# Kernel optimization log

Hardware: AMD Instinct MI355X
Metric: run time of the kernel (lower is better)

Reference implementation:

```python
import jax, jax.numpy as jnp
import numpy as np

N, K, M, DIM = 131072, 16, 128, 64


def setup_inputs() -> dict:
    key = jax.random.key(0)
    kx, ks, ka, kb = jax.random.split(key, 4)
    return {
        "x": jax.random.normal(kx, (N, DIM), dtype=jnp.float32),
        "s": jax.random.normal(ks, (K,), dtype=jnp.float32),
        "a": jax.random.normal(ka, (K, M, DIM), dtype=jnp.float32),
        "b": jax.random.normal(kb, (K, M), dtype=jnp.float32),
    }


def reference(x, s, a, b):
    # scores[k, n, m] = x[n, :] @ a[k, m, :] + b[k, m]  (batched GEMM over k)
    scores = jnp.einsum("nd,kmd->knm", x, a) + b[:, None, :]
    # per-expert logsumexp over the m affine pieces -> [k, n]
    lse = jax.nn.logsumexp(scores, axis=-1)
    # signed sum over experts -> [n]
    return jnp.einsum("k,kn->n", s, lse)
```

## Files before the change

kernel.cpp:

```cpp
#include <hip/hip_runtime.h>
#include <hip/hip_bf16.h>

#define NROWS 131072
#define KEXP 16
#define MPC 128
#define DIMD 64

typedef float f32x4  __attribute__((ext_vector_type(4)));
typedef float f32x16 __attribute__((ext_vector_type(16)));
typedef short s16x8  __attribute__((ext_vector_type(8)));

#define L2E 1.4426950408889634f
#define LN2 0.6931471805599453f

static __device__ inline unsigned int b2u(__hip_bfloat162 h) {
    union { __hip_bfloat162 h; unsigned int u; } c;
    c.h = h;
    return c.u;
}

static __device__ inline int4 cvt8s(float4 f0, float4 f1, float sc) {
    __hip_bfloat162 p0 = __float22bfloat162_rn(make_float2(f0.x * sc, f0.y * sc));
    __hip_bfloat162 p1 = __float22bfloat162_rn(make_float2(f0.z * sc, f0.w * sc));
    __hip_bfloat162 p2 = __float22bfloat162_rn(make_float2(f1.x * sc, f1.y * sc));
    __hip_bfloat162 p3 = __float22bfloat162_rn(make_float2(f1.z * sc, f1.w * sc));
    int4 pk;
    pk.x = (int)b2u(p0); pk.y = (int)b2u(p1); pk.z = (int)b2u(p2); pk.w = (int)b2u(p3);
    return pk;
}

static __device__ inline void async_copy16(const void* g, void* l) {
    __builtin_amdgcn_global_load_lds(
        (const __attribute__((address_space(1))) unsigned int*)g,
        (__attribute__((address_space(3))) unsigned int*)l, 16, 0, 0);
}

__global__ void prep_kernel(const float* __restrict__ a, const float* __restrict__ b,
                            short* __restrict__ abff) {
    const int u   = blockIdx.x * 256 + threadIdx.x;
    const int k   = u / 1280;
    const int rem = u - k * 1280;
    const int mt  = rem / 320;
    const int rc  = rem - mt * 320;
    const int c   = rc >> 6;
    const int ul  = rc & 63;
    int4 pk;
    if (c < 4) {
        const float* p = a + (size_t)(k * MPC + mt * 32 + (ul & 31)) * DIMD
                           + c * 16 + (ul >> 5) * 8;
        pk = cvt8s(*(const float4*)(p), *(const float4*)(p + 4), L2E);
    } else {
        pk.x = 0; pk.y = 0; pk.z = 0; pk.w = 0;
        if (ul < 32) {
            union { __hip_bfloat16 h; unsigned short us; } cv;
            cv.h = __float2bfloat16(b[k * MPC + mt * 32 + ul] * L2E);
            pk.x = (int)cv.us;
        }
    }
    *(int4*)(abff + (size_t)u * 8) = pk;
}

__global__ __launch_bounds__(256, 4)
void fused_kernel(const float* __restrict__ x, const float* __restrict__ s,
                  const short* __restrict__ abff, float* __restrict__ out) {
    __shared__ int4 abuf[2][1280];

    const int tid  = threadIdx.x;
    const int w    = tid >> 6;
    const int l    = tid & 63;
    const int ln   = l & 31;
    const int half = l >> 5;

    const int family = blockIdx.x & 3;
    const int r0w    = (blockIdx.x >> 2) * 256 + w * 64;

    union { int4 i; s16x8 v; } Bf[2][4];
#pragma unroll
    for (int nt = 0; nt < 2; ++nt)
#pragma unroll
        for (int c = 0; c < 4; ++c) {
            const float* gp = x + (size_t)(r0w + nt * 32 + ln) * DIMD + c * 16 + half * 8;
            float4 f0 = *(const float4*)(gp);
            float4 f1 = *(const float4*)(gp + 4);
            Bf[nt][c].i = cvt8s(f0, f1, 1.0f);
        }

    union { int4 i; s16x8 v; } Bones;
    Bones.i.x = (half == 0) ? 0x3F80 : 0;
    Bones.i.y = 0; Bones.i.z = 0; Bones.i.w = 0;

    {
        const short* src = abff + (size_t)(family * 4) * 10240;
#pragma unroll
        for (int i = 0; i < 5; ++i) {
            const int ch = w * 5 + i;
            async_copy16(src + ch * 512 + l * 8, (char*)&abuf[0][0] + ch * 1024);
        }
    }
    __syncthreads();

    float racc0 = 0.f, racc1 = 0.f;

    for (int k = 0; k < 4; ++k) {
        const int kf = family * 4 + k;
        const int kb = k & 1;

        if (k + 1 < 4) {
            const short* src = abff + (size_t)(kf + 1) * 10240;
#pragma unroll
            for (int i = 0; i < 5; ++i) {
                const int ch = w * 5 + i;
                async_copy16(src + ch * 512 + l * 8,
                             (char*)&abuf[kb ^ 1][0] + ch * 1024);
            }
        }

        const float sk2 = s[kf] * LN2;
        float esum0 = 0.f, esum1 = 0.f;

#pragma unroll
        for (int mt = 0; mt < 4; ++mt) {
            s16x8 Af[5];
#pragma unroll
            for (int c = 0; c < 5; ++c)
                Af[c] = *(const s16x8*)((const short*)&abuf[kb][0] + (mt * 5 + c) * 512 + l * 8);

            {
                f32x16 acc = {};
#pragma unroll
                for (int c = 0; c < 4; ++c)
                    acc = __builtin_amdgcn_mfma_f32_32x32x16_bf16(Af[c], Bf[0][c].v, acc, 0, 0, 0);
                acc = __builtin_amdgcn_mfma_f32_32x32x16_bf16(Af[4], Bones.v, acc, 0, 0, 0);
                float s0 = 0.f, s1 = 0.f, s2 = 0.f, s3 = 0.f;
#pragma unroll
                for (int r = 0; r < 4; ++r) {
                    s0 += __builtin_amdgcn_exp2f(acc[4 * r + 0]);
                    s1 += __builtin_amdgcn_exp2f(acc[4 * r + 1]);
                    s2 += __builtin_amdgcn_exp2f(acc[4 * r + 2]);
                    s3 += __builtin_amdgcn_exp2f(acc[4 * r + 3]);
                }
                esum0 += (s0 + s1) + (s2 + s3);
            }
            {
                f32x16 acc = {};
#pragma unroll
                for (int c = 0; c < 4; ++c)
                    acc = __builtin_amdgcn_mfma_f32_32x32x16_bf16(Af[c], Bf[1][c].v, acc, 0, 0, 0);
                acc = __builtin_amdgcn_mfma_f32_32x32x16_bf16(Af[4], Bones.v, acc, 0, 0, 0);
                float s0 = 0.f, s1 = 0.f, s2 = 0.f, s3 = 0.f;
#pragma unroll
                for (int r = 0; r < 4; ++r) {
                    s0 += __builtin_amdgcn_exp2f(acc[4 * r + 0]);
                    s1 += __builtin_amdgcn_exp2f(acc[4 * r + 1]);
                    s2 += __builtin_amdgcn_exp2f(acc[4 * r + 2]);
                    s3 += __builtin_amdgcn_exp2f(acc[4 * r + 3]);
                }
                esum1 += (s0 + s1) + (s2 + s3);
            }
        }

        float tot0 = esum0 + __shfl_xor(esum0, 32);
        float tot1 = esum1 + __shfl_xor(esum1, 32);
        racc0 = fmaf(sk2, __log2f(tot0), racc0);
        racc1 = fmaf(sk2, __log2f(tot1), racc1);

        __syncthreads();
    }

    atomicAdd(&out[r0w + half * 32 + ln], half ? racc1 : racc0);
}

extern "C" void kernel_launch(void* const* d_in, const int* in_sizes, int n_in,
                              void* d_out, int out_size, void* d_ws, size_t ws_size,
                              hipStream_t stream) {
    const float* x = (const float*)d_in[0];
    const float* s = (const float*)d_in[1];
    const float* a = (const float*)d_in[2];
    const float* b = (const float*)d_in[3];
    float* out = (float*)d_out;

    short* abff = (short*)d_ws;

    hipMemsetAsync(d_out, 0, (size_t)NROWS * sizeof(float), stream);
    prep_kernel<<<80, 256, 0, stream>>>(a, b, abff);
    fused_kernel<<<(NROWS / 256) * 4, 256, 0, stream>>>(x, s, abff, out);
}
```

Measured before the change: 124.1 us.

## Software-pipeline MFMA chains with exp2 reduction of previous tile

Restructures the inner expert loop so the exp2-sum epilogue of one 32x32 accumulator tile is issued alongside the MFMA chain for the next tile. Two accumulators are kept live in a ping-pong arrangement. The aim is to hide the exp/transcendental latency behind matrix-core work. Launch bounds drop from 4 to 3 waves per SIMD target to leave room for the extra accumulator registers, at the cost of lower occupancy.

```diff
diff --git a/kernel.cpp b/kernel.cpp
--- a/kernel.cpp
+++ b/kernel.cpp
@@ -35,6 +35,27 @@
         (__attribute__((address_space(3))) unsigned int*)l, 16, 0, 0);
 }
 
+static __device__ inline f32x16 mfma_chain5(const s16x8* Af, const s16x8* Bfv, s16x8 Bones) {
+    f32x16 acc = {};
+#pragma unroll
+    for (int c = 0; c < 4; ++c)
+        acc = __builtin_amdgcn_mfma_f32_32x32x16_bf16(Af[c], Bfv[c], acc, 0, 0, 0);
+    acc = __builtin_amdgcn_mfma_f32_32x32x16_bf16(Af[4], Bones, acc, 0, 0, 0);
+    return acc;
+}
+
+static __device__ inline float exp2sum16(f32x16 acc) {
+    float s0 = 0.f, s1 = 0.f, s2 = 0.f, s3 = 0.f;
+#pragma unroll
+    for (int r = 0; r < 4; ++r) {
+        s0 += __builtin_amdgcn_exp2f(acc[4 * r + 0]);
+        s1 += __builtin_amdgcn_exp2f(acc[4 * r + 1]);
+        s2 += __builtin_amdgcn_exp2f(acc[4 * r + 2]);
+        s3 += __builtin_amdgcn_exp2f(acc[4 * r + 3]);
+    }
+    return (s0 + s1) + (s2 + s3);
+}
+
 __global__ void prep_kernel(const float* __restrict__ a, const float* __restrict__ b,
                             short* __restrict__ abff) {
     const int u   = blockIdx.x * 256 + threadIdx.x;
@@ -60,7 +81,7 @@
     *(int4*)(abff + (size_t)u * 8) = pk;
 }
 
-__global__ __launch_bounds__(256, 4)
+__global__ __launch_bounds__(256, 3)
 void fused_kernel(const float* __restrict__ x, const float* __restrict__ s,
                   const short* __restrict__ abff, float* __restrict__ out) {
     __shared__ int4 abuf[2][1280];
@@ -74,15 +95,15 @@
     const int family = blockIdx.x & 3;
     const int r0w    = (blockIdx.x >> 2) * 256 + w * 64;
 
-    union { int4 i; s16x8 v; } Bf[2][4];
+    s16x8 Bfv[2][4];
 #pragma unroll
     for (int nt = 0; nt < 2; ++nt)
 #pragma unroll
         for (int c = 0; c < 4; ++c) {
             const float* gp = x + (size_t)(r0w + nt * 32 + ln) * DIMD + c * 16 + half * 8;
-            float4 f0 = *(const float4*)(gp);
-            float4 f1 = *(const float4*)(gp + 4);
-            Bf[nt][c].i = cvt8s(f0, f1, 1.0f);
+            union { int4 i; s16x8 v; } u;
+            u.i = cvt8s(*(const float4*)(gp), *(const float4*)(gp + 4), 1.0f);
+            Bfv[nt][c] = u.v;
         }
 
     union { int4 i; s16x8 v; } Bones;
@@ -116,51 +137,35 @@
         }
 
         const float sk2 = s[kf] * LN2;
-        float esum0 = 0.f, esum1 = 0.f;
+        const short* lbase = (const short*)&abuf[kb][0] + l * 8;
+
+        float  esum[2] = {0.f, 0.f};
+        f32x16 accP[2];
+        s16x8  Af[5];
 
 #pragma unroll
-        for (int mt = 0; mt < 4; ++mt) {
-            s16x8 Af[5];
+        for (int c = 0; c < 5; ++c)
+            Af[c] = *(const s16x8*)(lbase + c * 512);
+        accP[0] = mfma_chain5(Af, Bfv[0], Bones.v);
+
 #pragma unroll
-            for (int c = 0; c < 5; ++c)
-                Af[c] = *(const s16x8*)((const short*)&abuf[kb][0] + (mt * 5 + c) * 512 + l * 8);
+        for (int sidx = 1; sidx < 8; ++sidx) {
+            const int mt = sidx >> 1;
+            const int nt = sidx & 1;
+            if (nt == 0) {
+#pragma unroll
+                for (int c = 0; c < 5; ++c)
+                    Af[c] = *(const s16x8*)(lbase + (mt * 5 + c) * 512);
+            }
+            const int pp = (sidx - 1) & 1;
+            const float e = exp2sum16(accP[pp]);
+            accP[nt] = mfma_chain5(Af, Bfv[nt], Bones.v);
+            esum[pp] += e;
+        }
+        esum[1] += exp2sum16(accP[1]);
 
-            {
-                f32x16 acc = {};
-#pragma unroll
-                for (int c = 0; c < 4; ++c)
-                    acc = __builtin_amdgcn_mfma_f32_32x32x16_bf16(Af[c], Bf[0][c].v, acc, 0, 0, 0);
-                acc = __builtin_amdgcn_mfma_f32_32x32x16_bf16(Af[4], Bones.v, acc, 0, 0, 0);
-                float s0 = 0.f, s1 = 0.f, s2 = 0.f, s3 = 0.f;
-#pragma unroll
-                for (int r = 0; r < 4; ++r) {
-                    s0 += __builtin_amdgcn_exp2f(acc[4 * r + 0]);
-                    s1 += __builtin_amdgcn_exp2f(acc[4 * r + 1]);
-                    s2 += __builtin_amdgcn_exp2f(acc[4 * r + 2]);
-                    s3 += __builtin_amdgcn_exp2f(acc[4 * r + 3]);
-                }
-                esum0 += (s0 + s1) + (s2 + s3);
-            }
-            {
-                f32x16 acc = {};
-#pragma unroll
-                for (int c = 0; c < 4; ++c)
-                    acc = __builtin_amdgcn_mfma_f32_32x32x16_bf16(Af[c], Bf[1][c].v, acc, 0, 0, 0);
-                acc = __builtin_amdgcn_mfma_f32_32x32x16_bf16(Af[4], Bones.v, acc, 0, 0, 0);
-                float s0 = 0.f, s1 = 0.f, s2 = 0.f, s3 = 0.f;
-#pragma unroll
-                for (int r = 0; r < 4; ++r) {
-                    s0 += __builtin_amdgcn_exp2f(acc[4 * r + 0]);
-                    s1 += __builtin_amdgcn_exp2f(acc[4 * r + 1]);
-                    s2 += __builtin_amdgcn_exp2f(acc[4 * r + 2]);
-                    s3 += __builtin_amdgcn_exp2f(acc[4 * r + 3]);
-                }
-                esum1 += (s0 + s1) + (s2 + s3);
-            }
-        }
-
-        float tot0 = esum0 + __shfl_xor(esum0, 32);
-        float tot1 = esum1 + __shfl_xor(esum1, 32);
+        float tot0 = esum[0] + __shfl_xor(esum[0], 32);
+        float tot1 = esum[1] + __shfl_xor(esum[1], 32);
         racc0 = fmaf(sk2, __log2f(tot0), racc0);
         racc1 = fmaf(sk2, __log2f(tot1), racc1);
 
```

New measurement: 142.3 us. +14.6%, slower.
